# Kernel optimization log

Measured on AMD Instinct MI355X. Metric: run time of the kernel, lower is better.

## Reference

```python
import jax, jax.numpy as jnp
import numpy as np

COST_CLASS, COST_BBOX, COST_GIOU = 1.0, 5.0, 2.0


def box_cxcywh_to_xyxy(b):
    cx, cy, w, h = jnp.split(b, 4, axis=-1)
    return jnp.concatenate([cx - 0.5 * w, cy - 0.5 * h, cx + 0.5 * w, cy + 0.5 * h], axis=-1)


def generalized_box_iou(a, b):
    # a: [N,4] xyxy, b: [M,4] xyxy -> [N,M]
    area_a = (a[:, 2] - a[:, 0]) * (a[:, 3] - a[:, 1])
    area_b = (b[:, 2] - b[:, 0]) * (b[:, 3] - b[:, 1])
    lt = jnp.maximum(a[:, None, :2], b[None, :, :2])
    rb = jnp.minimum(a[:, None, 2:], b[None, :, 2:])
    wh = jnp.clip(rb - lt, 0.0)
    inter = wh[..., 0] * wh[..., 1]
    union = area_a[:, None] + area_b[None, :] - inter
    iou = inter / union
    lt2 = jnp.minimum(a[:, None, :2], b[None, :, :2])
    rb2 = jnp.maximum(a[:, None, 2:], b[None, :, 2:])
    wh2 = jnp.clip(rb2 - lt2, 0.0)
    encl = wh2[..., 0] * wh2[..., 1]
    return iou - (encl - union) / encl


@jax.jit
def _cost_matrix(pred_logits, pred_boxes, tgt_labels, tgt_boxes):
    bs, Q, _ = pred_logits.shape
    out_prob = jax.nn.softmax(pred_logits.reshape(bs * Q, -1), axis=-1)   # [bs*Q, C]
    out_bbox = pred_boxes.reshape(bs * Q, 4)                              # [bs*Q, 4]
    tgt_ids = tgt_labels.reshape(-1)                                      # [bs*T]
    tgt_bb = tgt_boxes.reshape(-1, 4)                                     # [bs*T, 4]
    cost_class = 1.0 - out_prob[:, tgt_ids]                               # [bs*Q, bs*T]
    cost_bbox = jnp.sum(jnp.abs(out_bbox[:, None, :] - tgt_bb[None, :, :]), axis=-1)  # L1 cdist
    cost_giou = 1.0 - generalized_box_iou(box_cxcywh_to_xyxy(out_bbox), box_cxcywh_to_xyxy(tgt_bb))
    C = COST_BBOX * cost_bbox + COST_CLASS * cost_class + COST_GIOU * cost_giou
    return C.reshape(bs, Q, -1)                                           # [bs, Q, bs*T]


def _lsa(cost):
    # Hungarian (shortest augmenting path / Jonker-Volgenant), cost: [n, m], n <= m.
    # Returns, for each row i, the assigned column (globally optimal assignment).
    n, m = cost.shape
    INF = 1e18
    u = np.zeros(n + 1)
    v = np.zeros(m + 1)
    p = np.zeros(m + 1, dtype=np.int64)    # p[j] = row matched to column j (1-indexed, 0 = free)
    way = np.zeros(m + 1, dtype=np.int64)
    for i in range(1, n + 1):
        p[0] = i
        j0 = 0
        minv = np.full(m + 1, INF)
        used = np.zeros(m + 1, dtype=bool)
        while True:
            used[j0] = True
            i0 = p[j0]
            cur = cost[i0 - 1] - u[i0] - v[1:]
            mask = ~used[1:]
            upd = mask & (cur < minv[1:])
            minv[1:] = np.where(upd, cur, minv[1:])
            way[1:] = np.where(upd, j0, way[1:])
            cand = np.where(mask, minv[1:], INF)
            j1 = int(np.argmin(cand)) + 1
            delta = cand[j1 - 1]
            u[p[used]] += delta
            v[used] -= delta
            minv[1:] = np.where(mask, minv[1:] - delta, minv[1:])
            j0 = j1
            if p[j0] == 0:
                break
        while j0:
            j1 = way[j0]
            p[j0] = p[j1]
            j0 = j1
    rows = np.zeros(n, dtype=np.int64)
    for j in range(1, m + 1):
        if p[j] > 0:
            rows[p[j] - 1] = j - 1
    return rows


def setup_inputs() -> dict:
    key = jax.random.key(0)
    k1, k2, k3, k4 = jax.random.split(key, 4)
    bs, Q, C, T = 32, 900, 91, 30
    return {
        'pred_logits': jax.random.normal(k1, (bs, Q, C), dtype=jnp.float32),
        'pred_boxes': jax.random.uniform(k2, (bs, Q, 4), dtype=jnp.float32),
        'tgt_labels': jax.random.randint(k3, (bs, T), 0, C),
        'tgt_boxes': jax.random.uniform(k4, (bs, T, 4), dtype=jnp.float32),
    }


def reference(pred_logits, pred_boxes, tgt_labels, tgt_boxes):
    C3 = _cost_matrix(pred_logits, pred_boxes, tgt_labels, tgt_boxes)  # [bs, Q, bs*T]
    bs, Q, _ = C3.shape
    T = tgt_labels.shape[1]
    C_np = np.asarray(jax.device_get(C3), dtype=np.float64)
    pred_idx = np.zeros((bs, T), dtype=np.int64)
    tgt_idx = np.zeros((bs, T), dtype=np.int64)
    for i in range(bs):
        c = C_np[i, :, i * T:(i + 1) * T]        # per-image block [Q, T] (== split-by-sizes)
        preds = _lsa(c.T)                        # for each target, matched prediction
        order = np.argsort(preds, kind='stable') # scipy returns row indices sorted ascending
        pred_idx[i] = preds[order]
        tgt_idx[i] = np.arange(T, dtype=np.int64)[order]
    return C3, jnp.asarray(pred_idx), jnp.asarray(tgt_idx)
```

## Files before the change

### kernel.cpp

```cpp
#include <hip/hip_runtime.h>
#include <math.h>

#define BS 32
#define NQ 900
#define NC 91
#define NT 30
#define NJ (BS*NT)
#define C3_SZ ((size_t)BS*NQ*NJ)
#define NROWS (BS*NQ)

#define LT 960
#define LWAVES (LT/64)
#define NCOSTBLK 224
#define MAXROWS 132

__device__ __forceinline__ float fast_rcp(float x) { return __builtin_amdgcn_rcpf(x); }

struct SharedLSA {
    float  cst[NT * NQ];
    double u[NT + 1];
    int    p[NQ + 1];
    int    way[NQ + 1];
    double red_v[LWAVES];
    int    red_i[LWAVES];
    int    rows[NT];
    int    tl[NT];
    float4 tbox[NT];
    float  rminv[NT];
    int    rminc[NT];
    int    aflag[NT + 1];
};
struct SharedCost {
    float  prob[MAXROWS][NC];
    float4 pbx[MAXROWS];
};

__device__ __forceinline__ float cost_elem(
    float pcx, float pcy, float pw, float ph,
    float px0, float py0, float px1, float py1, float area_a,
    float pr,
    float tcx, float tcy, float tw, float th,
    float tx0, float ty0, float tx1, float ty1, float area_b)
{
    float cost_bbox = fabsf(pcx - tcx) + fabsf(pcy - tcy) + fabsf(pw - tw) + fabsf(ph - th);
    float ix0 = fmaxf(px0, tx0), iy0 = fmaxf(py0, ty0);
    float ix1 = fminf(px1, tx1), iy1 = fminf(py1, ty1);
    float inter = fmaxf(ix1 - ix0, 0.f) * fmaxf(iy1 - iy0, 0.f);
    float uni = area_a + area_b - inter;
    float iou = inter * fast_rcp(uni);
    float ex0 = fminf(px0, tx0), ey0 = fminf(py0, ty0);
    float ex1 = fmaxf(px1, tx1), ey1 = fmaxf(py1, ty1);
    float encl = fmaxf(ex1 - ex0, 0.f) * fmaxf(ey1 - ey0, 0.f);
    float giou = iou - (encl - uni) * fast_rcp(encl);
    return 5.0f * cost_bbox - pr - 2.0f * giou + 3.0f;
}

__device__ __forceinline__ void softmax_prob_row(const float* __restrict__ lrow, int lane,
                                                 float* __restrict__ prob)
{
    float a = (lane < NC)      ? lrow[lane]      : -1e30f;
    float c = (lane + 64 < NC) ? lrow[lane + 64] : -1e30f;
    float m = fmaxf(a, c);
    for (int off = 32; off; off >>= 1) m = fmaxf(m, __shfl_xor(m, off));
    float ea = (lane < NC)      ? __expf(a - m) : 0.f;
    float ec = (lane + 64 < NC) ? __expf(c - m) : 0.f;
    float s = ea + ec;
    for (int off = 32; off; off >>= 1) s += __shfl_xor(s, off);
    float rs = fast_rcp(s);
    if (lane < NC)      prob[lane]      = ea * rs;
    if (lane + 64 < NC) prob[lane + 64] = ec * rs;
}

__global__ __launch_bounds__(LT) void fused_kernel(
    const float* __restrict__ logits,
    const float* __restrict__ pboxes,
    const int*   __restrict__ tlabels,
    const float* __restrict__ tboxes,
    float* __restrict__ out,
    float* __restrict__ outp,
    float* __restrict__ outt)
{
    __shared__ union { SharedLSA l; SharedCost c; } sm;
    const int t = threadIdx.x;
    const int wv = t >> 6;
    const int lane = t & 63;

    if (blockIdx.x < BS) {
        const int b = blockIdx.x;
        const float* lg  = logits + (size_t)b * NQ * NC;
        const float* pbx = pboxes + (size_t)b * NQ * 4;

        if (t < NT) {
            sm.l.tl[t] = tlabels[b * NT + t];
            sm.l.tbox[t] = ((const float4*)tboxes)[b * NT + t];
        }
        for (int j = t; j <= NQ; j += LT) { sm.l.p[j] = 0; sm.l.way[j] = 0; }
        __syncthreads();

        for (int q = wv; q < NQ; q += LWAVES) {
            const float* lrow = lg + (size_t)q * NC;
            float a = (lane < NC)      ? lrow[lane]      : -1e30f;
            float c = (lane + 64 < NC) ? lrow[lane + 64] : -1e30f;
            float m = fmaxf(a, c);
            for (int off = 32; off; off >>= 1) m = fmaxf(m, __shfl_xor(m, off));
            float ea = (lane < NC)      ? __expf(a - m) : 0.f;
            float ec = (lane + 64 < NC) ? __expf(c - m) : 0.f;
            float s = ea + ec;
            for (int off = 32; off; off >>= 1) s += __shfl_xor(s, off);
            float rs = fast_rcp(s);

            int lbl = sm.l.tl[lane < NT ? lane : 0];
            float pa = __shfl(ea, lbl & 63);
            float pc = __shfl(ec, lbl & 63);
            if (lane < NT) {
                float pr = ((lbl < 64) ? pa : pc) * rs;
                float4 pb = ((const float4*)pbx)[q];
                float pcx = pb.x, pcy = pb.y, pw = pb.z, ph = pb.w;
                float px0 = pcx - 0.5f*pw, py0 = pcy - 0.5f*ph;
                float px1 = pcx + 0.5f*pw, py1 = pcy + 0.5f*ph;
                float area_a = pw * ph;
                float4 tb = sm.l.tbox[lane];
                float tcx = tb.x, tcy = tb.y, tw = tb.z, th = tb.w;
                float tx0 = tcx - 0.5f*tw, ty0 = tcy - 0.5f*th;
                float tx1 = tcx + 0.5f*tw, ty1 = tcy + 0.5f*th;
                float area_b = tw * th;
                sm.l.cst[lane * NQ + q] =
                    cost_elem(pcx, pcy, pw, ph, px0, py0, px1, py1, area_a,
                              pr, tcx, tcy, tw, th, tx0, ty0, tx1, ty1, area_b);
            }
        }
        __syncthreads();

        for (int r = wv; r < NT; r += LWAVES) {
            float bv = 1e30f; int bi = 1 << 20;
            for (int j = lane; j < NQ; j += 64) {
                float v = sm.l.cst[r * NQ + j];
                if (v < bv) { bv = v; bi = j; }
            }
            for (int off = 32; off; off >>= 1) {
                float ov = __shfl_xor(bv, off);
                int   oi = __shfl_xor(bi, off);
                if (ov < bv || (ov == bv && oi < bi)) { bv = ov; bi = oi; }
            }
            if (lane == 0) { sm.l.rminv[r] = bv; sm.l.rminc[r] = bi + 1; }
        }
        __syncthreads();

        if (wv == 0) {
            int r = lane;
            int myc = (r < NT) ? sm.l.rminc[r] : -1;
            bool win = (r < NT);
            for (int j = 0; j < NT; ++j) {
                int cj = __shfl(myc, j);
                if (j < r && cj == myc) win = false;
            }
            if (r < NT) {
                sm.l.u[r + 1] = (double)sm.l.rminv[r];
                sm.l.aflag[r + 1] = win ? 1 : 0;
                if (win) sm.l.p[myc] = r + 1;
            }
        }
        double v_t = 0.0;
        __syncthreads();

        for (int i = 1; i <= NT; ++i) {
            if (sm.l.aflag[i]) continue;
            double minv_t = 1e18;
            bool used_t = (t == 0);
            int p_t = (t == 0) ? i : ((t <= NQ) ? sm.l.p[t] : 0);
            int i0 = i, j0 = 0, j1f = 0;
            for (;;) {
                double u_i0 = sm.l.u[i0];
                double cand; int ci;
                if (t >= 1 && t <= NQ && !used_t) {
                    double cur = ((double)sm.l.cst[(i0 - 1) * NQ + (t - 1)] - u_i0) - v_t;
                    if (cur < minv_t) { minv_t = cur; sm.l.way[t] = j0; }
                    cand = minv_t; ci = t;
                } else { cand = 1e18; ci = 1 << 20; }
                for (int off = 32; off; off >>= 1) {
                    double ov = __shfl_xor(cand, off);
                    int    oi = __shfl_xor(ci, off);
                    if (ov < cand || (ov == cand && oi < ci)) { cand = ov; ci = oi; }
                }
                if (lane == 0) { sm.l.red_v[wv] = cand; sm.l.red_i[wv] = ci; }
                __syncthreads();
                double rv; int ri;
                if (lane < LWAVES) { rv = sm.l.red_v[lane]; ri = sm.l.red_i[lane]; }
                else               { rv = 1e18;             ri = 1 << 20; }
                for (int off = 8; off; off >>= 1) {
                    double ov = __shfl_xor(rv, off);
                    int    oi = __shfl_xor(ri, off);
                    if (ov < rv || (ov == rv && oi < ri)) { rv = ov; ri = oi; }
                }
                double delta = __shfl(rv, 0);
                int    j1    = __shfl(ri, 0);
                if (used_t) { v_t -= delta; sm.l.u[p_t] += delta; }
                else if (t >= 1 && t <= NQ) minv_t -= delta;
                if (t == j1) { used_t = true; p_t = sm.l.p[j1]; }
                int pj1 = sm.l.p[j1];
                __syncthreads();
                if (pj1 == 0) { j1f = j1; break; }
                i0 = pj1; j0 = j1;
            }
            if (t == 0) {
                int j0w = j1f;
                while (j0w) {
                    int jp = sm.l.way[j0w];
                    sm.l.p[j0w] = (jp == 0) ? i : sm.l.p[jp];
                    j0w = jp;
                }
            }
            __syncthreads();
        }
        if (t >= 1 && t <= NQ && sm.l.p[t] > 0) sm.l.rows[sm.l.p[t] - 1] = t - 1;
        __syncthreads();

        if (wv == 0) {
            int k = lane;
            int key = (k < NT) ? sm.l.rows[k] : 0x7fffffff;
            int rank = 0;
            for (int j = 0; j < NT; ++j) {
                int kj = __shfl(key, j);
                if (kj < key) ++rank;
            }
            if (k < NT) {
                outp[b * NT + rank] = (float)key;
                outt[b * NT + rank] = (float)k;
            }
        }
    } else {
        const int cb = blockIdx.x - BS;
        const int r0 = (int)(((long long)cb * NROWS) / NCOSTBLK);
        const int r1 = (int)(((long long)(cb + 1) * NROWS) / NCOSTBLK);
        const int nrows = r1 - r0;

        for (int rr = wv; rr < nrows; rr += LWAVES)
            softmax_prob_row(logits + (size_t)(r0 + rr) * NC, lane, sm.c.prob[rr]);
        for (int rr = t; rr < nrows; rr += LT)
            sm.c.pbx[rr] = ((const float4*)pboxes)[r0 + rr];

        const int   lbl = tlabels[t];
        const float4 tb = ((const float4*)tboxes)[t];
        const float tcx = tb.x, tcy = tb.y, tw = tb.z, th = tb.w;
        const float tx0 = tcx - 0.5f*tw, ty0 = tcy - 0.5f*th;
        const float tx1 = tcx + 0.5f*tw, ty1 = tcy + 0.5f*th;
        const float area_b = tw * th;
        __syncthreads();

        float* op = out + (size_t)r0 * NJ + t;
        #pragma unroll 2
        for (int rr = 0; rr < nrows; ++rr) {
            float pr = sm.c.prob[rr][lbl];
            float4 pb = sm.c.pbx[rr];
            float pcx = pb.x, pcy = pb.y, pw = pb.z, ph = pb.w;
            float px0 = pcx - 0.5f*pw, py0 = pcy - 0.5f*ph;
            float px1 = pcx + 0.5f*pw, py1 = pcy + 0.5f*ph;
            float area_a = pw * ph;
            float v = cost_elem(pcx, pcy, pw, ph, px0, py0, px1, py1, area_a,
                                pr, tcx, tcy, tw, th, tx0, ty0, tx1, ty1, area_b);
            __builtin_nontemporal_store(v, op);
            op += NJ;
        }
    }
}

extern "C" void kernel_launch(void* const* d_in, const int* in_sizes, int n_in,
                              void* d_out, int out_size, void* d_ws, size_t ws_size,
                              hipStream_t stream) {
    const float* logits  = (const float*)d_in[0];
    const float* pboxes  = (const float*)d_in[1];
    const int*   tlabels = (const int*)d_in[2];
    const float* tboxes  = (const float*)d_in[3];
    float* out = (float*)d_out;

    fused_kernel<<<BS + NCOSTBLK, LT, 0, stream>>>(
        logits, pboxes, tlabels, tboxes,
        out, out + C3_SZ, out + C3_SZ + (size_t)BS * NT);
}
```

Baseline: 184.4 us.

## Have LSA blocks consume diagonal cost blocks from cost blocks via flags

The LSA blocks no longer recompute softmax and costs for their own image's diagonal block. Cost blocks first write the diagonal entries, publish them through per-image atomic counters, then write the off-diagonal entries. The LSA blocks spin on those counters and load the diagonal block from global memory. This removes redundant softmax work in the serial LSA blocks, but it adds inter-block spin-waiting, a memset launch, and the risk of deadlock if cost blocks are not co-resident with the waiting LSA blocks.

```diff
diff --git a/kernel.cpp b/kernel.cpp
--- a/kernel.cpp
+++ b/kernel.cpp
@@ -24,8 +24,6 @@
     double red_v[LWAVES];
     int    red_i[LWAVES];
     int    rows[NT];
-    int    tl[NT];
-    float4 tbox[NT];
     float  rminv[NT];
     int    rminc[NT];
     int    aflag[NT + 1];
@@ -78,56 +76,103 @@
     const float* __restrict__ tboxes,
     float* __restrict__ out,
     float* __restrict__ outp,
-    float* __restrict__ outt)
+    float* __restrict__ outt,
+    int*   __restrict__ flags)
 {
     __shared__ union { SharedLSA l; SharedCost c; } sm;
     const int t = threadIdx.x;
     const int wv = t >> 6;
     const int lane = t & 63;
 
-    if (blockIdx.x < BS) {
+    if (blockIdx.x >= BS) {
+        const int cb = blockIdx.x - BS;
+        const int r0 = (int)(((long long)cb * NROWS) / NCOSTBLK);
+        const int r1 = (int)(((long long)(cb + 1) * NROWS) / NCOSTBLK);
+        const int nrows = r1 - r0;
+
+        for (int rr = wv; rr < nrows; rr += LWAVES)
+            softmax_prob_row(logits + (size_t)(r0 + rr) * NC, lane, sm.c.prob[rr]);
+        for (int rr = t; rr < nrows; rr += LT)
+            sm.c.pbx[rr] = ((const float4*)pboxes)[r0 + rr];
+        __syncthreads();
+
+        for (int e = t; e < nrows * NT; e += LT) {
+            int rr  = e / NT;
+            int r   = e - rr * NT;
+            int row = r0 + rr;
+            int bb  = row / NQ;
+            int col = bb * NT + r;
+            float pr = sm.c.prob[rr][tlabels[col]];
+            float4 pb = sm.c.pbx[rr];
+            float pcx = pb.x, pcy = pb.y, pw = pb.z, ph = pb.w;
+            float px0 = pcx - 0.5f*pw, py0 = pcy - 0.5f*ph;
+            float px1 = pcx + 0.5f*pw, py1 = pcy + 0.5f*ph;
+            float area_a = pw * ph;
+            float4 tb2 = ((const float4*)tboxes)[col];
+            float tcx = tb2.x, tcy = tb2.y, tw = tb2.z, th = tb2.w;
+            float tx0 = tcx - 0.5f*tw, ty0 = tcy - 0.5f*th;
+            float tx1 = tcx + 0.5f*tw, ty1 = tcy + 0.5f*th;
+            float area_b = tw * th;
+            out[(size_t)row * NJ + col] =
+                cost_elem(pcx, pcy, pw, ph, px0, py0, px1, py1, area_a,
+                          pr, tcx, tcy, tw, th, tx0, ty0, tx1, ty1, area_b);
+        }
+        __syncthreads();
+        if (t == 0) {
+            __threadfence();
+            int b_lo = r0 / NQ, b_hi = (r1 - 1) / NQ;
+            for (int bb = b_lo; bb <= b_hi; ++bb)
+                atomicAdd(&flags[bb], 1);
+        }
+
+        const int   lbl = tlabels[t];
+        const float4 tb = ((const float4*)tboxes)[t];
+        const float tcx = tb.x, tcy = tb.y, tw = tb.z, th = tb.w;
+        const float tx0 = tcx - 0.5f*tw, ty0 = tcy - 0.5f*th;
+        const float tx1 = tcx + 0.5f*tw, ty1 = tcy + 0.5f*th;
+        const float area_b = tw * th;
+        const unsigned drow0 = (unsigned)((t / NT) * NQ);
+
+        float* op = out + (size_t)r0 * NJ + t;
+        #pragma unroll 2
+        for (int rr = 0; rr < nrows; ++rr) {
+            const int row = r0 + rr;
+            float pr = sm.c.prob[rr][lbl];
+            float4 pb = sm.c.pbx[rr];
+            float pcx = pb.x, pcy = pb.y, pw = pb.z, ph = pb.w;
+            float px0 = pcx - 0.5f*pw, py0 = pcy - 0.5f*ph;
+            float px1 = pcx + 0.5f*pw, py1 = pcy + 0.5f*ph;
+            float area_a = pw * ph;
+            float v = cost_elem(pcx, pcy, pw, ph, px0, py0, px1, py1, area_a,
+                                pr, tcx, tcy, tw, th, tx0, ty0, tx1, ty1, area_b);
+            if ((unsigned)row - drow0 >= (unsigned)NQ)
+                __builtin_nontemporal_store(v, op);
+            op += NJ;
+        }
+    } else {
         const int b = blockIdx.x;
-        const float* lg  = logits + (size_t)b * NQ * NC;
-        const float* pbx = pboxes + (size_t)b * NQ * 4;
-
-        if (t < NT) {
-            sm.l.tl[t] = tlabels[b * NT + t];
-            sm.l.tbox[t] = ((const float4*)tboxes)[b * NT + t];
-        }
+
         for (int j = t; j <= NQ; j += LT) { sm.l.p[j] = 0; sm.l.way[j] = 0; }
-        __syncthreads();
-
-        for (int q = wv; q < NQ; q += LWAVES) {
-            const float* lrow = lg + (size_t)q * NC;
-            float a = (lane < NC)      ? lrow[lane]      : -1e30f;
-            float c = (lane + 64 < NC) ? lrow[lane + 64] : -1e30f;
-            float m = fmaxf(a, c);
-            for (int off = 32; off; off >>= 1) m = fmaxf(m, __shfl_xor(m, off));
-            float ea = (lane < NC)      ? __expf(a - m) : 0.f;
-            float ec = (lane + 64 < NC) ? __expf(c - m) : 0.f;
-            float s = ea + ec;
-            for (int off = 32; off; off >>= 1) s += __shfl_xor(s, off);
-            float rs = fast_rcp(s);
-
-            int lbl = sm.l.tl[lane < NT ? lane : 0];
-            float pa = __shfl(ea, lbl & 63);
-            float pc = __shfl(ec, lbl & 63);
-            if (lane < NT) {
-                float pr = ((lbl < 64) ? pa : pc) * rs;
-                float4 pb = ((const float4*)pbx)[q];
-                float pcx = pb.x, pcy = pb.y, pw = pb.z, ph = pb.w;
-                float px0 = pcx - 0.5f*pw, py0 = pcy - 0.5f*ph;
-                float px1 = pcx + 0.5f*pw, py1 = pcy + 0.5f*ph;
-                float area_a = pw * ph;
-                float4 tb = sm.l.tbox[lane];
-                float tcx = tb.x, tcy = tb.y, tw = tb.z, th = tb.w;
-                float tx0 = tcx - 0.5f*tw, ty0 = tcy - 0.5f*th;
-                float tx1 = tcx + 0.5f*tw, ty1 = tcy + 0.5f*th;
-                float area_b = tw * th;
-                sm.l.cst[lane * NQ + q] =
-                    cost_elem(pcx, pcy, pw, ph, px0, py0, px1, py1, area_a,
-                              pr, tcx, tcy, tw, th, tx0, ty0, tx1, ty1, area_b);
-            }
+
+        int exp_cnt = 0;
+        for (int cb = 0; cb < NCOSTBLK; ++cb) {
+            int a0 = (int)(((long long)cb * NROWS) / NCOSTBLK);
+            int a1 = (int)(((long long)(cb + 1) * NROWS) / NCOSTBLK);
+            if (a0 < (b + 1) * NQ && a1 > b * NQ) ++exp_cnt;
+        }
+        if (t == 0) {
+            while (__hip_atomic_load(&flags[b], __ATOMIC_ACQUIRE,
+                                     __HIP_MEMORY_SCOPE_AGENT) < exp_cnt)
+                __builtin_amdgcn_s_sleep(2);
+        }
+        __syncthreads();
+        __threadfence();
+
+        const float* src = out + (size_t)b * NQ * NJ + (size_t)b * NT;
+        for (int e = t; e < NT * NQ; e += LT) {
+            int q = e / NT;
+            int r = e - q * NT;
+            sm.l.cst[r * NQ + q] = src[(size_t)q * NJ + r];
         }
         __syncthreads();
 
@@ -228,39 +273,6 @@
                 outt[b * NT + rank] = (float)k;
             }
         }
-    } else {
-        const int cb = blockIdx.x - BS;
-        const int r0 = (int)(((long long)cb * NROWS) / NCOSTBLK);
-        const int r1 = (int)(((long long)(cb + 1) * NROWS) / NCOSTBLK);
-        const int nrows = r1 - r0;
-
-        for (int rr = wv; rr < nrows; rr += LWAVES)
-            softmax_prob_row(logits + (size_t)(r0 + rr) * NC, lane, sm.c.prob[rr]);
-        for (int rr = t; rr < nrows; rr += LT)
-            sm.c.pbx[rr] = ((const float4*)pboxes)[r0 + rr];
-
-        const int   lbl = tlabels[t];
-        const float4 tb = ((const float4*)tboxes)[t];
-        const float tcx = tb.x, tcy = tb.y, tw = tb.z, th = tb.w;
-        const float tx0 = tcx - 0.5f*tw, ty0 = tcy - 0.5f*th;
-        const float tx1 = tcx + 0.5f*tw, ty1 = tcy + 0.5f*th;
-        const float area_b = tw * th;
-        __syncthreads();
-
-        float* op = out + (size_t)r0 * NJ + t;
-        #pragma unroll 2
-        for (int rr = 0; rr < nrows; ++rr) {
-            float pr = sm.c.prob[rr][lbl];
-            float4 pb = sm.c.pbx[rr];
-            float pcx = pb.x, pcy = pb.y, pw = pb.z, ph = pb.w;
-            float px0 = pcx - 0.5f*pw, py0 = pcy - 0.5f*ph;
-            float px1 = pcx + 0.5f*pw, py1 = pcy + 0.5f*ph;
-            float area_a = pw * ph;
-            float v = cost_elem(pcx, pcy, pw, ph, px0, py0, px1, py1, area_a,
-                                pr, tcx, tcy, tw, th, tx0, ty0, tx1, ty1, area_b);
-            __builtin_nontemporal_store(v, op);
-            op += NJ;
-        }
     }
 }
 
@@ -271,9 +283,11 @@
     const float* pboxes  = (const float*)d_in[1];
     const int*   tlabels = (const int*)d_in[2];
     const float* tboxes  = (const float*)d_in[3];
-    float* out = (float*)d_out;
-
+    float* out  = (float*)d_out;
+    int* flags  = (int*)d_ws;
+
+    hipMemsetAsync(flags, 0, BS * sizeof(int), stream);
     fused_kernel<<<BS + NCOSTBLK, LT, 0, stream>>>(
         logits, pboxes, tlabels, tboxes,
-        out, out + C3_SZ, out + C3_SZ + (size_t)BS * NT);
-}
+        out, out + C3_SZ, out + C3_SZ + (size_t)BS * NT, flags);
+}
```

Result: slower. 200.9 us (+8.9%).

## Stage logits through shared memory in chunks and compute per-row softmax stats separately

Applied to the files above, without the earlier changes.

The LSA blocks now copy logits in coalesced chunks of 60 rows into shared memory. One thread per row computes the max and reciprocal sum serially, and the target-label logits are gathered into the cost buffer. A second pass assigns one thread per query to compute all 30 cost elements from the staged logit, replacing the earlier wave-per-query loop that left most lanes idle. It adds 15 chunk barriers, serial per-row reductions done by only 60 threads, and more shared memory use.

```diff
diff --git a/kernel.cpp b/kernel.cpp
--- a/kernel.cpp
+++ b/kernel.cpp
@@ -13,11 +13,15 @@
 #define LWAVES (LT/64)
 #define NCOSTBLK 224
 #define MAXROWS 132
+#define RCH 60
 
 __device__ __forceinline__ float fast_rcp(float x) { return __builtin_amdgcn_rcpf(x); }
 
 struct SharedLSA {
     float  cst[NT * NQ];
+    float  mx[NQ];
+    float  rs[NQ];
+    float  stage[RCH * NC];
     double u[NT + 1];
     int    p[NQ + 1];
     int    way[NQ + 1];
@@ -95,36 +99,49 @@
             sm.l.tbox[t] = ((const float4*)tboxes)[b * NT + t];
         }
         for (int j = t; j <= NQ; j += LT) { sm.l.p[j] = 0; sm.l.way[j] = 0; }
-        __syncthreads();
-
-        for (int q = wv; q < NQ; q += LWAVES) {
-            const float* lrow = lg + (size_t)q * NC;
-            float a = (lane < NC)      ? lrow[lane]      : -1e30f;
-            float c = (lane + 64 < NC) ? lrow[lane + 64] : -1e30f;
-            float m = fmaxf(a, c);
-            for (int off = 32; off; off >>= 1) m = fmaxf(m, __shfl_xor(m, off));
-            float ea = (lane < NC)      ? __expf(a - m) : 0.f;
-            float ec = (lane + 64 < NC) ? __expf(c - m) : 0.f;
-            float s = ea + ec;
-            for (int off = 32; off; off >>= 1) s += __shfl_xor(s, off);
-            float rs = fast_rcp(s);
-
-            int lbl = sm.l.tl[lane < NT ? lane : 0];
-            float pa = __shfl(ea, lbl & 63);
-            float pc = __shfl(ec, lbl & 63);
-            if (lane < NT) {
-                float pr = ((lbl < 64) ? pa : pc) * rs;
-                float4 pb = ((const float4*)pbx)[q];
-                float pcx = pb.x, pcy = pb.y, pw = pb.z, ph = pb.w;
-                float px0 = pcx - 0.5f*pw, py0 = pcy - 0.5f*ph;
-                float px1 = pcx + 0.5f*pw, py1 = pcy + 0.5f*ph;
-                float area_a = pw * ph;
-                float4 tb = sm.l.tbox[lane];
+
+        for (int ch = 0; ch < NQ / RCH; ++ch) {
+            const int base = ch * RCH;
+            for (int e = t; e < RCH * NC; e += LT)
+                sm.l.stage[e] = lg[(size_t)base * NC + e];
+            __syncthreads();
+            if (t < RCH) {
+                const float* row = &sm.l.stage[t * NC];
+                float m = row[0];
+                #pragma unroll 10
+                for (int c2 = 1; c2 < NC; ++c2) m = fmaxf(m, row[c2]);
+                float s = 0.f;
+                #pragma unroll 7
+                for (int c2 = 0; c2 < NC; ++c2) s += __expf(row[c2] - m);
+                sm.l.mx[base + t] = m;
+                sm.l.rs[base + t] = fast_rcp(s);
+            }
+            for (int e = t; e < RCH * NT; e += LT) {
+                int lq = e % RCH;
+                int r  = e / RCH;
+                sm.l.cst[r * NQ + base + lq] = sm.l.stage[lq * NC + sm.l.tl[r]];
+            }
+            __syncthreads();
+        }
+
+        if (t < NQ) {
+            const int q = t;
+            float4 pb = ((const float4*)pbx)[q];
+            float pcx = pb.x, pcy = pb.y, pw = pb.z, ph = pb.w;
+            float px0 = pcx - 0.5f*pw, py0 = pcy - 0.5f*ph;
+            float px1 = pcx + 0.5f*pw, py1 = pcy + 0.5f*ph;
+            float area_a = pw * ph;
+            float mxq = sm.l.mx[q], rsq = sm.l.rs[q];
+            #pragma unroll 5
+            for (int r = 0; r < NT; ++r) {
+                float lv = sm.l.cst[r * NQ + q];
+                float pr = __expf(lv - mxq) * rsq;
+                float4 tb = sm.l.tbox[r];
                 float tcx = tb.x, tcy = tb.y, tw = tb.z, th = tb.w;
                 float tx0 = tcx - 0.5f*tw, ty0 = tcy - 0.5f*th;
                 float tx1 = tcx + 0.5f*tw, ty1 = tcy + 0.5f*th;
                 float area_b = tw * th;
-                sm.l.cst[lane * NQ + q] =
+                sm.l.cst[r * NQ + q] =
                     cost_elem(pcx, pcy, pw, ph, px0, py0, px1, py1, area_a,
                               pr, tcx, tcy, tw, th, tx0, ty0, tx1, ty1, area_b);
             }
```

New measurement: 243.1 us. 31.9% more time.

## Run Hungarian augmenting loop in a single wavefront to eliminate block barriers

Applied to the files above, without the earlier changes.

The shortest-augmenting-path phase moves from all 960 threads with two block-wide barriers per step to a single 64-lane wavefront. Each lane keeps 15 columns of minv in registers, and the v potentials move to shared memory. This removes the cross-wave reduction and __syncthreads latency on every augmentation step, at the cost of each lane doing 15x more serial column work. The other 14 waves sit idle during this phase, and shared-memory read-after-write within the wave relies on lockstep execution.

```diff
diff --git a/kernel.cpp b/kernel.cpp
--- a/kernel.cpp
+++ b/kernel.cpp
@@ -13,16 +13,16 @@
 #define LWAVES (LT/64)
 #define NCOSTBLK 224
 #define MAXROWS 132
+#define KPL 15
 
 __device__ __forceinline__ float fast_rcp(float x) { return __builtin_amdgcn_rcpf(x); }
 
 struct SharedLSA {
     float  cst[NT * NQ];
     double u[NT + 1];
+    double vv[NQ + 1];
     int    p[NQ + 1];
     int    way[NQ + 1];
-    double red_v[LWAVES];
-    int    red_i[LWAVES];
     int    rows[NT];
     int    tl[NT];
     float4 tbox[NT];
@@ -94,7 +94,7 @@
             sm.l.tl[t] = tlabels[b * NT + t];
             sm.l.tbox[t] = ((const float4*)tboxes)[b * NT + t];
         }
-        for (int j = t; j <= NQ; j += LT) { sm.l.p[j] = 0; sm.l.way[j] = 0; }
+        for (int j = t; j <= NQ; j += LT) { sm.l.p[j] = 0; sm.l.way[j] = 0; sm.l.vv[j] = 0.0; }
         __syncthreads();
 
         for (int q = wv; q < NQ; q += LWAVES) {
@@ -147,71 +147,79 @@
         __syncthreads();
 
         if (wv == 0) {
-            int r = lane;
-            int myc = (r < NT) ? sm.l.rminc[r] : -1;
-            bool win = (r < NT);
-            for (int j = 0; j < NT; ++j) {
-                int cj = __shfl(myc, j);
-                if (j < r && cj == myc) win = false;
-            }
-            if (r < NT) {
-                sm.l.u[r + 1] = (double)sm.l.rminv[r];
-                sm.l.aflag[r + 1] = win ? 1 : 0;
-                if (win) sm.l.p[myc] = r + 1;
-            }
-        }
-        double v_t = 0.0;
-        __syncthreads();
-
-        for (int i = 1; i <= NT; ++i) {
-            if (sm.l.aflag[i]) continue;
-            double minv_t = 1e18;
-            bool used_t = (t == 0);
-            int p_t = (t == 0) ? i : ((t <= NQ) ? sm.l.p[t] : 0);
-            int i0 = i, j0 = 0, j1f = 0;
-            for (;;) {
-                double u_i0 = sm.l.u[i0];
-                double cand; int ci;
-                if (t >= 1 && t <= NQ && !used_t) {
-                    double cur = ((double)sm.l.cst[(i0 - 1) * NQ + (t - 1)] - u_i0) - v_t;
-                    if (cur < minv_t) { minv_t = cur; sm.l.way[t] = j0; }
-                    cand = minv_t; ci = t;
-                } else { cand = 1e18; ci = 1 << 20; }
-                for (int off = 32; off; off >>= 1) {
-                    double ov = __shfl_xor(cand, off);
-                    int    oi = __shfl_xor(ci, off);
-                    if (ov < cand || (ov == cand && oi < ci)) { cand = ov; ci = oi; }
-                }
-                if (lane == 0) { sm.l.red_v[wv] = cand; sm.l.red_i[wv] = ci; }
-                __syncthreads();
-                double rv; int ri;
-                if (lane < LWAVES) { rv = sm.l.red_v[lane]; ri = sm.l.red_i[lane]; }
-                else               { rv = 1e18;             ri = 1 << 20; }
-                for (int off = 8; off; off >>= 1) {
-                    double ov = __shfl_xor(rv, off);
-                    int    oi = __shfl_xor(ri, off);
-                    if (ov < rv || (ov == rv && oi < ri)) { rv = ov; ri = oi; }
-                }
-                double delta = __shfl(rv, 0);
-                int    j1    = __shfl(ri, 0);
-                if (used_t) { v_t -= delta; sm.l.u[p_t] += delta; }
-                else if (t >= 1 && t <= NQ) minv_t -= delta;
-                if (t == j1) { used_t = true; p_t = sm.l.p[j1]; }
-                int pj1 = sm.l.p[j1];
-                __syncthreads();
-                if (pj1 == 0) { j1f = j1; break; }
-                i0 = pj1; j0 = j1;
-            }
-            if (t == 0) {
-                int j0w = j1f;
-                while (j0w) {
-                    int jp = sm.l.way[j0w];
-                    sm.l.p[j0w] = (jp == 0) ? i : sm.l.p[jp];
-                    j0w = jp;
-                }
-            }
-            __syncthreads();
-        }
+            {
+                int r = lane;
+                int myc = (r < NT) ? sm.l.rminc[r] : -1;
+                bool win = (r < NT);
+                for (int j = 0; j < NT; ++j) {
+                    int cj = __shfl(myc, j);
+                    if (j < r && cj == myc) win = false;
+                }
+                if (r < NT) {
+                    sm.l.u[r + 1] = (double)sm.l.rminv[r];
+                    sm.l.aflag[r + 1] = win ? 1 : 0;
+                    if (win) sm.l.p[myc] = r + 1;
+                }
+            }
+
+            double minv[KPL];
+            for (int i = 1; i <= NT; ++i) {
+                if (sm.l.aflag[i]) continue;
+                #pragma unroll
+                for (int k = 0; k < KPL; ++k) minv[k] = 1e18;
+                unsigned usedm = 0;
+                int i0 = i, j0 = 0, j1f = 0;
+                for (;;) {
+                    double u_i0 = sm.l.u[i0];
+                    double best = 1e18; int bestc = 1 << 20;
+                    #pragma unroll
+                    for (int k = 0; k < KPL; ++k) {
+                        int col = 1 + lane + (k << 6);
+                        if (col <= NQ && !((usedm >> k) & 1u)) {
+                            double cur = (double)sm.l.cst[(i0 - 1) * NQ + (col - 1)]
+                                         - u_i0 - sm.l.vv[col];
+                            if (cur < minv[k]) { minv[k] = cur; sm.l.way[col] = j0; }
+                            if (minv[k] < best) { best = minv[k]; bestc = col; }
+                        }
+                    }
+                    for (int off = 32; off; off >>= 1) {
+                        double ov = __shfl_xor(best, off);
+                        int    oc = __shfl_xor(bestc, off);
+                        if (ov < best || (ov == best && oc < bestc)) { best = ov; bestc = oc; }
+                    }
+                    double delta = best;
+                    int    j1    = bestc;
+                    if (lane == 0) sm.l.u[i] += delta;
+                    #pragma unroll
+                    for (int k = 0; k < KPL; ++k) {
+                        int col = 1 + lane + (k << 6);
+                        if (col <= NQ) {
+                            if ((usedm >> k) & 1u) {
+                                sm.l.vv[col] -= delta;
+                                sm.l.u[sm.l.p[col]] += delta;
+                            } else {
+                                minv[k] -= delta;
+                            }
+                        }
+                    }
+                    if (((j1 - 1) & 63) == lane)
+                        usedm |= (1u << ((j1 - 1) >> 6));
+                    int pj1 = sm.l.p[j1];
+                    if (pj1 == 0) { j1f = j1; break; }
+                    i0 = pj1; j0 = j1;
+                }
+                if (lane == 0) {
+                    int j0w = j1f;
+                    while (j0w) {
+                        int jp = sm.l.way[j0w];
+                        sm.l.p[j0w] = (jp == 0) ? i : sm.l.p[jp];
+                        j0w = jp;
+                    }
+                }
+            }
+        }
+        __syncthreads();
+
         if (t >= 1 && t <= NQ && sm.l.p[t] > 0) sm.l.rows[sm.l.p[t] - 1] = t - 1;
         __syncthreads();
 
```

Result: slower. 190.1 us (+3.1%).
